# Performance work log

Measured on AMD Instinct MI355X. Metric: run time of the kernel, lower is better.

## Reference

```python
import jax, jax.numpy as jnp
import numpy as np

LN_EPS = 1e-5

def _layernorm(x, g, b):
    mu = jnp.mean(x, axis=-1, keepdims=True)
    var = jnp.mean(jnp.square(x - mu), axis=-1, keepdims=True)
    return (x - mu) * jax.lax.rsqrt(var + LN_EPS) * g + b

def setup_inputs() -> dict:
    key = jax.random.key(0)
    ks = jax.random.split(key, 8)
    B, T, C = 4, 2048, 1024
    s = 0.02
    return {
        "x": jax.random.normal(ks[0], (B, T, C), jnp.float32),
        "w_qkv": jax.random.normal(ks[1], (C, 3 * C), jnp.float32) * s,
        "b_qkv": jnp.zeros((3 * C,), jnp.float32),
        "w_out": jax.random.normal(ks[2], (C, C), jnp.float32) * s,
        "b_out": jnp.zeros((C,), jnp.float32),
        "w1": jax.random.normal(ks[3], (C, 4 * C), jnp.float32) * s,
        "b1": jnp.zeros((4 * C,), jnp.float32),
        "w2": jax.random.normal(ks[4], (4 * C, C), jnp.float32) * s,
        "b2": jnp.zeros((C,), jnp.float32),
        "g1": jnp.ones((C,), jnp.float32),
        "be1": jnp.zeros((C,), jnp.float32),
        "g2": jnp.ones((C,), jnp.float32),
        "be2": jnp.zeros((C,), jnp.float32),
        "n_head": 16,
    }

def reference(x, w_qkv, b_qkv, w_out, b_out, w1, b1, w2, b2, g1, be1, g2, be2, n_head):
    B, T, C = x.shape
    H = n_head
    D = C // H
    # --- causal self-attention ---
    qkv = x @ w_qkv + b_qkv                      # [B,T,3C]
    q, k, v = jnp.split(qkv, 3, axis=-1)
    q = q.reshape(B, T, H, D).transpose(0, 2, 1, 3)  # [B,H,T,D]
    k = k.reshape(B, T, H, D).transpose(0, 2, 1, 3)
    v = v.reshape(B, T, H, D).transpose(0, 2, 1, 3)
    attn = jnp.einsum("bhqd,bhkd->bhqk", q, k) * (1.0 / np.sqrt(D))
    causal = jnp.tril(jnp.ones((T, T), bool))
    attn = jnp.where(causal, attn, jnp.float32(-jnp.inf))
    attn = jax.nn.softmax(attn, axis=-1)
    y = jnp.einsum("bhqk,bhkd->bhqd", attn, v)
    y = y.transpose(0, 2, 1, 3).reshape(B, T, C)
    y = y @ w_out + b_out
    # post-norm residual (norm applied to sublayer output)
    x = x + _layernorm(y, g1, be1)
    # --- MLP ---
    h = jax.nn.gelu(x @ w1 + b1, approximate=False)
    h = h @ w2 + b2
    x = x + _layernorm(h, g2, be2)
    return x
```

## Files before the change

### kernel.cpp

```cpp
#include <hip/hip_runtime.h>
#include <hip/hip_bf16.h>

typedef unsigned short ushort_t;
using bf16x8 = __attribute__((ext_vector_type(8))) short;
using f32x4  = __attribute__((ext_vector_type(4))) float;

#define DEV __device__ __forceinline__

DEV unsigned short f2bf(float f) {
    unsigned int u = __builtin_bit_cast(unsigned int, f);
    u = (u + 0x7fffu + ((u >> 16) & 1u)) >> 16;
    return (unsigned short)u;
}

DEV int cvtpk_bf16(float lo, float hi) {
    int r;
    asm("v_cvt_pk_bf16_f32 %0, %1, %2" : "=v"(r) : "v"(lo), "v"(hi));
    return r;
}

DEV void gload16(const unsigned short* g, unsigned short* l) {
    __builtin_amdgcn_global_load_lds(
        (const __attribute__((address_space(1))) void*)g,
        (__attribute__((address_space(3))) void*)l, 16, 0, 0);
}

DEV float gelu_f(float v) {
    float u = v * (0.79788456f + 0.03567741f * v * v);
    float t = __builtin_amdgcn_exp2f(u * 2.88539008f);
    return v * t * __builtin_amdgcn_rcpf(t + 1.0f);
}

__global__ __launch_bounds__(256) void cvtbf_kernel(const float* __restrict__ in,
                                                    unsigned short* __restrict__ out) {
    int i = (blockIdx.x * 256 + threadIdx.x) * 4;
    float4 v = *(const float4*)&in[i];
    out[i + 0] = f2bf(v.x);
    out[i + 1] = f2bf(v.y);
    out[i + 2] = f2bf(v.z);
    out[i + 3] = f2bf(v.w);
}

__global__ __launch_bounds__(256) void transpose_cvt_kernel(const float* __restrict__ in,
                                                            unsigned short* __restrict__ out,
                                                            int R, int C) {
    __shared__ float t[32][33];
    int tx = threadIdx.x, ty = threadIdx.y;
    int c0 = blockIdx.x * 32, r0 = blockIdx.y * 32;
#pragma unroll
    for (int i = 0; i < 4; ++i)
        t[ty + i * 8][tx] = in[(size_t)(r0 + ty + i * 8) * C + c0 + tx];
    __syncthreads();
#pragma unroll
    for (int i = 0; i < 4; ++i)
        out[(size_t)(c0 + ty + i * 8) * R + r0 + tx] = f2bf(t[tx][ty + i * 8]);
}

__global__ __launch_bounds__(256) void vtrans_kernel(const unsigned short* __restrict__ qkvb,
                                                     unsigned short* __restrict__ vtg) {
    __shared__ unsigned short t[64 * 66];
    const int tid = threadIdx.x;
    const int t0 = blockIdx.x * 64;
    const int bh = blockIdx.y;
    const int b = bh >> 4, h = bh & 15;
    const unsigned short* src = qkvb + (size_t)(b * 2048 + t0) * 3072 + 2048 + h * 64;
#pragma unroll
    for (int c = 0; c < 2; ++c) {
        int cid = c * 256 + tid;
        int row = cid >> 3, cc = cid & 7;
        *(int4*)&t[row * 66 + cc * 8] = *(const int4*)&src[(size_t)row * 3072 + cc * 8];
    }
    __syncthreads();
    unsigned short* dst = vtg + (size_t)bh * 64 * 2048 + t0;
#pragma unroll
    for (int c = 0; c < 2; ++c) {
        int cid = c * 256 + tid;
        int d = cid >> 3, cc2 = cid & 7;
        bf16x8 v;
#pragma unroll
        for (int j = 0; j < 8; ++j) v[j] = (short)t[(cc2 * 8 + j) * 66 + d];
        *(bf16x8*)&dst[(size_t)d * 2048 + cc2 * 8] = v;
    }
}

template <int ACT, int OBF>
__global__ __launch_bounds__(512, 2) void gemm256_kernel(
    const unsigned short* __restrict__ A, const unsigned short* __restrict__ Bt,
    const float* __restrict__ bias, void* __restrict__ out,
    int N, int K, int gridNt) {
    __shared__ __align__(16) unsigned short lA[2][256 * 64];
    __shared__ __align__(16) unsigned short lB[2][256 * 64];
    const int tid = threadIdx.x;
    const int lane = tid & 63, wid = tid >> 6;
    const int g = lane >> 4, lr = lane & 15;
    const int wm = wid >> 2, wn = wid & 3;

    const int nwg = gridDim.x, cpx = nwg >> 3, bid = blockIdx.x;
    const int wkid = (bid & 7) * cpx + (bid >> 3);
    const int mt = wkid / gridNt, nt = wkid % gridNt;
    const int m0 = mt * 256, n0 = nt * 256;

    auto stageA = [&](int s, int kt, int bb) {
        int c = s * 512 + tid;
        int row = c & 255, kb = c >> 8;
        gload16(&A[(size_t)(m0 + row) * K + kt * 64 + kb * 8],
                &lA[bb][(size_t)(s * 512 + (tid & ~63)) * 8]);
    };
    auto stageB = [&](int s, int kt, int bb) {
        int c = s * 512 + tid;
        int row = c & 255, kb = c >> 8;
        gload16(&Bt[(size_t)(n0 + row) * K + kt * 64 + kb * 8],
                &lB[bb][(size_t)(s * 512 + (tid & ~63)) * 8]);
    };

    f32x4 acc[8][4] = {};
    bf16x8 bfr[4];
    const int nkt = K >> 6;

    stageA(0, 0, 0); stageA(1, 0, 0); stageB(0, 0, 0); stageB(1, 0, 0);
    stageA(2, 0, 0); stageA(3, 0, 0); stageB(2, 0, 0); stageB(3, 0, 0);
    asm volatile("s_waitcnt vmcnt(4)" ::: "memory");
    __builtin_amdgcn_s_barrier();
    asm volatile("" ::: "memory");

    for (int kt = 0; kt < nkt; ++kt) {
        const int buf = kt & 1;
        const bool more = (kt + 1 < nkt);
#pragma unroll
        for (int p = 0; p < 4; ++p) {
            const int ks = p >> 1, mh = p & 1;
            bf16x8 af[4];
#pragma unroll
            for (int mf2 = 0; mf2 < 4; ++mf2) {
                int c = (ks * 4 + g) * 256 + wm * 128 + (mh * 4 + mf2) * 16 + lr;
                af[mf2] = *(const bf16x8*)&lA[buf][(size_t)c * 8];
            }
            if (mh == 0) {
#pragma unroll
                for (int nf = 0; nf < 4; ++nf) {
                    int c = (ks * 4 + g) * 256 + wn * 64 + nf * 16 + lr;
                    bfr[nf] = *(const bf16x8*)&lB[buf][(size_t)c * 8];
                }
            }
            if (more) {
                if (p == 0)      { stageA(0, kt + 1, buf ^ 1); stageA(1, kt + 1, buf ^ 1); }
                else if (p == 1) { stageB(0, kt + 1, buf ^ 1); stageB(1, kt + 1, buf ^ 1); }
                else if (p == 2) { stageA(2, kt + 1, buf ^ 1); stageA(3, kt + 1, buf ^ 1); }
                else             { stageB(2, kt + 1, buf ^ 1); stageB(3, kt + 1, buf ^ 1); }
            }
            __builtin_amdgcn_s_barrier();
            asm volatile("s_waitcnt lgkmcnt(0)" ::: "memory");
            __builtin_amdgcn_sched_barrier(0);
            __builtin_amdgcn_s_setprio(1);
#pragma unroll
            for (int mf2 = 0; mf2 < 4; ++mf2)
#pragma unroll
                for (int nf = 0; nf < 4; ++nf)
                    acc[mh * 4 + mf2][nf] = __builtin_amdgcn_mfma_f32_16x16x32_bf16(
                        af[mf2], bfr[nf], acc[mh * 4 + mf2][nf], 0, 0, 0);
            __builtin_amdgcn_s_setprio(0);
            __builtin_amdgcn_sched_barrier(0);
            if (p == 1) {
                if (more) asm volatile("s_waitcnt vmcnt(4)" ::: "memory");
                else      asm volatile("s_waitcnt vmcnt(0)" ::: "memory");
            } else if (p == 3) {
                if (more) asm volatile("s_waitcnt vmcnt(4)" ::: "memory");
            }
            __builtin_amdgcn_s_barrier();
            asm volatile("" ::: "memory");
        }
    }

#pragma unroll
    for (int mf = 0; mf < 8; ++mf) {
#pragma unroll
        for (int nf = 0; nf < 4; ++nf) {
            int col = n0 + wn * 64 + nf * 16 + lr;
            float bv = bias[col];
#pragma unroll
            for (int r = 0; r < 4; ++r) {
                int row = m0 + wm * 128 + mf * 16 + g * 4 + r;
                float v = acc[mf][nf][r] + bv;
                if (ACT == 1) v = gelu_f(v);
                if (OBF)
                    ((unsigned short*)out)[(size_t)row * N + col] = f2bf(v);
                else
                    ((float*)out)[(size_t)row * N + col] = v;
            }
        }
    }
}

template <int ACT, int OBF>
__global__ __launch_bounds__(512, 2) void gemm128_kernel(
    const unsigned short* __restrict__ A, const unsigned short* __restrict__ Bt,
    const float* __restrict__ bias, void* __restrict__ out,
    int N, int K, int gridNt) {
    __shared__ __align__(16) unsigned short lA[2][128 * 64];
    __shared__ __align__(16) unsigned short lB[2][256 * 64];
    const int tid = threadIdx.x;
    const int lane = tid & 63, wid = tid >> 6;
    const int g = lane >> 4, lr = lane & 15;
    const int wm = wid >> 2, wn = wid & 3;

    const int nwg = gridDim.x, cpx = nwg >> 3, bid = blockIdx.x;
    const int wkid = (bid & 7) * cpx + (bid >> 3);
    const int mt = wkid / gridNt, nt = wkid % gridNt;
    const int m0 = mt * 128, n0 = nt * 256;

    auto stageA = [&](int s, int kt, int bb) {
        int c = s * 512 + tid;
        int row = c & 127, kb = c >> 7;
        gload16(&A[(size_t)(m0 + row) * K + kt * 64 + kb * 8],
                &lA[bb][(size_t)(s * 512 + (tid & ~63)) * 8]);
    };
    auto stageB = [&](int s, int kt, int bb) {
        int c = s * 512 + tid;
        int row = c & 255, kb = c >> 8;
        gload16(&Bt[(size_t)(n0 + row) * K + kt * 64 + kb * 8],
                &lB[bb][(size_t)(s * 512 + (tid & ~63)) * 8]);
    };

    f32x4 acc[4][4] = {};
    const int nkt = K >> 6;

    stageA(0, 0, 0); stageB(0, 0, 0); stageB(1, 0, 0);
    stageA(1, 0, 0); stageB(2, 0, 0); stageB(3, 0, 0);
    asm volatile("s_waitcnt vmcnt(3)" ::: "memory");
    __builtin_amdgcn_s_barrier();
    asm volatile("" ::: "memory");

    for (int kt = 0; kt < nkt; ++kt) {
        const int buf = kt & 1;
        const bool more = (kt + 1 < nkt);
#pragma unroll
        for (int ks = 0; ks < 2; ++ks) {
            bf16x8 af[4], bfr[4];
#pragma unroll
            for (int mf = 0; mf < 4; ++mf) {
                int c = (ks * 4 + g) * 128 + wm * 64 + mf * 16 + lr;
                af[mf] = *(const bf16x8*)&lA[buf][(size_t)c * 8];
            }
#pragma unroll
            for (int nf = 0; nf < 4; ++nf) {
                int c = (ks * 4 + g) * 256 + wn * 64 + nf * 16 + lr;
                bfr[nf] = *(const bf16x8*)&lB[buf][(size_t)c * 8];
            }
            if (more) {
                if (ks == 0) { stageA(0, kt + 1, buf ^ 1); stageB(0, kt + 1, buf ^ 1); stageB(1, kt + 1, buf ^ 1); }
                else         { stageA(1, kt + 1, buf ^ 1); stageB(2, kt + 1, buf ^ 1); stageB(3, kt + 1, buf ^ 1); }
            }
            __builtin_amdgcn_s_barrier();
            asm volatile("s_waitcnt lgkmcnt(0)" ::: "memory");
            __builtin_amdgcn_sched_barrier(0);
            __builtin_amdgcn_s_setprio(1);
#pragma unroll
            for (int mf = 0; mf < 4; ++mf)
#pragma unroll
                for (int nf = 0; nf < 4; ++nf)
                    acc[mf][nf] = __builtin_amdgcn_mfma_f32_16x16x32_bf16(
                        af[mf], bfr[nf], acc[mf][nf], 0, 0, 0);
            __builtin_amdgcn_s_setprio(0);
            __builtin_amdgcn_sched_barrier(0);
            if (ks == 0) {
                if (more) asm volatile("s_waitcnt vmcnt(3)" ::: "memory");
                else      asm volatile("s_waitcnt vmcnt(0)" ::: "memory");
            } else {
                if (more) asm volatile("s_waitcnt vmcnt(3)" ::: "memory");
            }
            __builtin_amdgcn_s_barrier();
            asm volatile("" ::: "memory");
        }
    }

#pragma unroll
    for (int mf = 0; mf < 4; ++mf) {
#pragma unroll
        for (int nf = 0; nf < 4; ++nf) {
            int col = n0 + wn * 64 + nf * 16 + lr;
            float bv = bias[col];
#pragma unroll
            for (int r = 0; r < 4; ++r) {
                int row = m0 + wm * 64 + mf * 16 + g * 4 + r;
                float v = acc[mf][nf][r] + bv;
                if (ACT == 1) v = gelu_f(v);
                if (OBF)
                    ((unsigned short*)out)[(size_t)row * N + col] = f2bf(v);
                else
                    ((float*)out)[(size_t)row * N + col] = v;
            }
        }
    }
}

__global__ __launch_bounds__(256) void attn_kernel(const unsigned short* __restrict__ qkv,
                                                   const unsigned short* __restrict__ vtg,
                                                   unsigned short* __restrict__ y) {
    __shared__ unsigned short Kl[2][4096];
    __shared__ unsigned short Vl[2][4096];
    const int tid = threadIdx.x, lane = tid & 63, w = tid >> 6;
    const int g = lane >> 4, lr = lane & 15;
    const int p = blockIdx.x, h = blockIdx.y, b = blockIdx.z;
    const int bh = b * 16 + h;
    const size_t rs3 = 3072;
    const unsigned short* qbase = qkv + (size_t)b * 2048 * rs3 + h * 64;
    const unsigned short* kbase = qbase + 1024;
    const unsigned short* vbase = vtg + (size_t)bh * 64 * 2048;

    int ksoff[2], vsoff[2], ldoff[2];
#pragma unroll
    for (int c = 0; c < 2; ++c) {
        int row = w * 16 + c * 8 + (lane >> 3);
        int ccs = (lane & 7) ^ (row & 7) ^ (row >> 3);
        ksoff[c] = row * 3072 + ccs * 8;
        vsoff[c] = row * 2048 + ccs * 8;
        ldoff[c] = (w * 16 + c * 8) * 64;
    }

    const int idxP0 = 4 * (32 * (g & 1) + lr);
    const int idxP1 = idxP0 + 64;
    int idxA[4];
#pragma unroll
    for (int r = 0; r < 4; ++r) idxA[r] = 4 * (g * 20 + r);
    const bool ghigh = (g >> 1) != 0;
    const float qscale = 0.125f * 1.44269504089f;

    auto process = [&](int J) {
        const int q0w = J * 128 + w * 32;
        const int ktend = 2 * J + 2;
#pragma unroll
        for (int c = 0; c < 2; ++c) {
            gload16(&kbase[ksoff[c]], &Kl[0][ldoff[c]]);
            gload16(&vbase[vsoff[c]], &Vl[0][ldoff[c]]);
        }
        int qf[2][2][4];
#pragma unroll
        for (int sub = 0; sub < 2; ++sub)
#pragma unroll
            for (int f = 0; f < 2; ++f) {
                int4 v = *(const int4*)&qbase[(size_t)(q0w + sub * 16 + lr) * rs3 + f * 32 + g * 8];
                int vv[4] = {v.x, v.y, v.z, v.w};
#pragma unroll
                for (int i = 0; i < 4; ++i) {
                    unsigned int u = (unsigned int)vv[i];
                    float lo = __builtin_bit_cast(float, u << 16) * qscale;
                    float hi = __builtin_bit_cast(float, u & 0xffff0000u) * qscale;
                    qf[sub][f][i] = cvtpk_bf16(lo, hi);
                }
            }

        f32x4 O[2][4] = {};
        float m_[2] = {-3.0e38f, -3.0e38f}, l_[2] = {0.f, 0.f};

        int buf = 0;
        for (int kt = 0; kt < ktend; ++kt) {
            asm volatile("s_waitcnt vmcnt(0)" ::: "memory");
            __builtin_amdgcn_s_barrier();
            asm volatile("" ::: "memory");
            if (kt + 1 < ktend) {
#pragma unroll
                for (int c = 0; c < 2; ++c) {
                    gload16(&kbase[(size_t)(kt + 1) * 64 * 3072 + ksoff[c]], &Kl[buf ^ 1][ldoff[c]]);
                    gload16(&vbase[vsoff[c] + (kt + 1) * 64], &Vl[buf ^ 1][ldoff[c]]);
                }
            }
            const unsigned short* Kc = Kl[buf];
            const unsigned short* Vc = Vl[buf];

            const bool act0 = (kt * 64) <= (q0w + 15);
            const bool act1 = (kt * 64) <= (q0w + 31);

            f32x4 s0[4], s1[4];
#pragma unroll
            for (int st = 0; st < 4; ++st) {
                int rbase = (st * 16 + lr) * 64;
                int sw = (lr & 7) ^ (st * 2 + (lr >> 3));
                bf16x8 kf0 = *(const bf16x8*)&Kc[rbase + ((g ^ sw) * 8)];
                bf16x8 kf1 = *(const bf16x8*)&Kc[rbase + (((4 + g) ^ sw) * 8)];
                if (act0) {
                    f32x4 a = {};
                    a = __builtin_amdgcn_mfma_f32_16x16x32_bf16(kf0, *(const bf16x8*)&qf[0][0], a, 0, 0, 0);
                    a = __builtin_amdgcn_mfma_f32_16x16x32_bf16(kf1, *(const bf16x8*)&qf[0][1], a, 0, 0, 0);
                    s0[st] = a;
                }
                if (act1) {
                    f32x4 a = {};
                    a = __builtin_amdgcn_mfma_f32_16x16x32_bf16(kf0, *(const bf16x8*)&qf[1][0], a, 0, 0, 0);
                    a = __builtin_amdgcn_mfma_f32_16x16x32_bf16(kf1, *(const bf16x8*)&qf[1][1], a, 0, 0, 0);
                    s1[st] = a;
                }
            }

            int wt0[2][4], wt1[2][4];
#pragma unroll
            for (int sub = 0; sub < 2; ++sub) {
                if (sub == 0 && !act0) continue;
                if (sub == 1 && !act1) continue;
                f32x4* s = (sub == 0) ? s0 : s1;
                const int qmin = q0w + sub * 16;
                if (kt * 64 + 63 > qmin) {
                    int qv = qmin + lr;
#pragma unroll
                    for (int st = 0; st < 4; ++st) {
                        int keyb = kt * 64 + st * 16 + g * 4;
#pragma unroll
                        for (int r = 0; r < 4; ++r)
                            if (keyb + r > qv) s[st][r] = -3.0e38f;
                    }
                }
                float mx = fmaxf(fmaxf(s[0][0], s[0][1]), fmaxf(s[0][2], s[0][3]));
#pragma unroll
                for (int st = 1; st < 4; ++st)
                    mx = fmaxf(mx, fmaxf(fmaxf(s[st][0], s[st][1]), fmaxf(s[st][2], s[st][3])));
                mx = fmaxf(mx, __shfl_xor(mx, 16));
                mx = fmaxf(mx, __shfl_xor(mx, 32));
                float mold = m_[sub];
                float mnew = fmaxf(mold, mx);
                float alpha = __builtin_amdgcn_exp2f(mold - mnew);
                m_[sub] = mnew;
                float rs = 0.f;
#pragma unroll
                for (int st = 0; st < 4; ++st)
#pragma unroll
                    for (int r = 0; r < 4; ++r) {
                        float pp = __builtin_amdgcn_exp2f(s[st][r] - mnew);
                        s[st][r] = pp;
                        rs += pp;
                    }
                rs += __shfl_xor(rs, 16);
                rs += __shfl_xor(rs, 32);
                l_[sub] = l_[sub] * alpha + rs;
                int av = __builtin_bit_cast(int, alpha);
                f32x4* Os = O[sub];
#pragma unroll
                for (int r = 0; r < 4; ++r) {
                    float ar = __builtin_bit_cast(float, __builtin_amdgcn_ds_bpermute(idxA[r], av));
#pragma unroll
                    for (int dt = 0; dt < 4; ++dt) Os[dt][r] *= ar;
                }
                int ws_[4][2];
#pragma unroll
                for (int st = 0; st < 4; ++st) {
                    ws_[st][0] = cvtpk_bf16(s[st][0], s[st][1]);
                    ws_[st][1] = cvtpk_bf16(s[st][2], s[st][3]);
                }
                int(*wt)[4] = (sub == 0) ? wt0 : wt1;
#pragma unroll
                for (int ks = 0; ks < 2; ++ks)
#pragma unroll
                    for (int hp = 0; hp < 4; ++hp) {
                        int idx = (hp < 2) ? idxP0 : idxP1;
                        int v0 = __builtin_amdgcn_ds_bpermute(idx, ws_[2 * ks][hp & 1]);
                        int v1 = __builtin_amdgcn_ds_bpermute(idx, ws_[2 * ks + 1][hp & 1]);
                        wt[ks][hp] = ghigh ? v1 : v0;
                    }
            }

#pragma unroll
            for (int ks = 0; ks < 2; ++ks) {
                bf16x8 pa0 = *(const bf16x8*)&wt0[ks][0];
                bf16x8 pa1 = *(const bf16x8*)&wt1[ks][0];
#pragma unroll
                for (int dt = 0; dt < 4; ++dt) {
                    int d = dt * 16 + lr;
                    int xv = (ks * 4 + g) ^ (lr & 7) ^ (dt * 2 + (lr >> 3));
                    bf16x8 vf = *(const bf16x8*)&Vc[d * 64 + xv * 8];
                    if (act0) O[0][dt] = __builtin_amdgcn_mfma_f32_16x16x32_bf16(pa0, vf, O[0][dt], 0, 0, 0);
                    if (act1) O[1][dt] = __builtin_amdgcn_mfma_f32_16x16x32_bf16(pa1, vf, O[1][dt], 0, 0, 0);
                }
            }
            buf ^= 1;
        }

#pragma unroll
        for (int sub = 0; sub < 2; ++sub) {
            int lv = __builtin_bit_cast(int, l_[sub]);
#pragma unroll
            for (int r = 0; r < 4; ++r) {
                float lval = __builtin_bit_cast(float, __builtin_amdgcn_ds_bpermute(idxA[r], lv));
                float inv = __builtin_amdgcn_rcpf(lval);
                int q = q0w + sub * 16 + g * 4 + r;
#pragma unroll
                for (int dt = 0; dt < 4; ++dt)
                    y[(size_t)(b * 2048 + q) * 1024 + h * 64 + dt * 16 + lr] =
                        f2bf(O[sub][dt][r] * inv);
            }
        }
    };

    process(15 - p);
    __syncthreads();
    process(p);
}

template <int WRITE_BF>
__global__ __launch_bounds__(256) void ln_kernel(const float* __restrict__ base,
                                                 const float* __restrict__ delta,
                                                 const float* __restrict__ gw,
                                                 const float* __restrict__ bw,
                                                 float* __restrict__ outf,
                                                 unsigned short* __restrict__ outb) {
    const int row = blockIdx.x;
    const int tid = threadIdx.x;
    const float* d = delta + (size_t)row * 1024;
    const float* bs = base + (size_t)row * 1024;
    float4 x = *(const float4*)&d[tid * 4];
    float s = x.x + x.y + x.z + x.w;
    float s2 = x.x * x.x + x.y * x.y + x.z * x.z + x.w * x.w;
#pragma unroll
    for (int off = 1; off < 64; off <<= 1) {
        s += __shfl_xor(s, off);
        s2 += __shfl_xor(s2, off);
    }
    __shared__ float red[8];
    if ((tid & 63) == 0) {
        red[tid >> 6] = s;
        red[4 + (tid >> 6)] = s2;
    }
    __syncthreads();
    s = red[0] + red[1] + red[2] + red[3];
    s2 = red[4] + red[5] + red[6] + red[7];
    float mu = s * (1.f / 1024.f);
    float var = s2 * (1.f / 1024.f) - mu * mu;
    float rsig = rsqrtf(var + 1e-5f);
    float4 bb = *(const float4*)&bs[tid * 4];
    float4 gv = *(const float4*)&gw[tid * 4];
    float4 bv = *(const float4*)&bw[tid * 4];
    float4 o;
    o.x = bb.x + (x.x - mu) * rsig * gv.x + bv.x;
    o.y = bb.y + (x.y - mu) * rsig * gv.y + bv.y;
    o.z = bb.z + (x.z - mu) * rsig * gv.z + bv.z;
    o.w = bb.w + (x.w - mu) * rsig * gv.w + bv.w;
    *(float4*)&outf[(size_t)row * 1024 + tid * 4] = o;
    if (WRITE_BF) {
        unsigned short* ob = outb + (size_t)row * 1024 + tid * 4;
        ob[0] = f2bf(o.x);
        ob[1] = f2bf(o.y);
        ob[2] = f2bf(o.z);
        ob[3] = f2bf(o.w);
    }
}

extern "C" void kernel_launch(void* const* d_in, const int* in_sizes, int n_in,
                              void* d_out, int out_size, void* d_ws, size_t ws_size,
                              hipStream_t stream) {
    const float* x = (const float*)d_in[0];
    const float* w_qkv = (const float*)d_in[1];
    const float* b_qkv = (const float*)d_in[2];
    const float* w_out = (const float*)d_in[3];
    const float* b_out = (const float*)d_in[4];
    const float* w1 = (const float*)d_in[5];
    const float* b1 = (const float*)d_in[6];
    const float* w2 = (const float*)d_in[7];
    const float* b2 = (const float*)d_in[8];
    const float* g1 = (const float*)d_in[9];
    const float* be1 = (const float*)d_in[10];
    const float* g2 = (const float*)d_in[11];
    const float* be2 = (const float*)d_in[12];

    const size_t MB = 1ull << 20;
    if (ws_size < 184 * MB) return;
    char* ws = (char*)d_ws;
    unsigned short* xb    = (unsigned short*)(ws + 0);
    unsigned short* vtg   = (unsigned short*)(ws + 0);
    unsigned short* wqkvt = (unsigned short*)(ws + 16 * MB);
    unsigned short* qkvb  = (unsigned short*)(ws + 22 * MB);
    unsigned short* hb    = (unsigned short*)(ws + 0);
    unsigned short* woutt = (unsigned short*)(ws + 70 * MB);
    unsigned short* yb    = (unsigned short*)(ws + 72 * MB);
    float*          attnp = (float*)(ws + 88 * MB);
    float*          ff    = (float*)(ws + 88 * MB);
    float*          x2f   = (float*)(ws + 120 * MB);
    unsigned short* x2b   = (unsigned short*)(ws + 152 * MB);
    unsigned short* w1t   = (unsigned short*)(ws + 168 * MB);
    unsigned short* w2t   = (unsigned short*)(ws + 176 * MB);

    cvtbf_kernel<<<8192, 256, 0, stream>>>(x, xb);
    transpose_cvt_kernel<<<dim3(96, 32), dim3(32, 8), 0, stream>>>(w_qkv, wqkvt, 1024, 3072);
    transpose_cvt_kernel<<<dim3(32, 32), dim3(32, 8), 0, stream>>>(w_out, woutt, 1024, 1024);
    transpose_cvt_kernel<<<dim3(128, 32), dim3(32, 8), 0, stream>>>(w1, w1t, 1024, 4096);
    transpose_cvt_kernel<<<dim3(32, 128), dim3(32, 8), 0, stream>>>(w2, w2t, 4096, 1024);
    gemm256_kernel<0, 1><<<384, 512, 0, stream>>>(xb, wqkvt, b_qkv, qkvb, 3072, 1024, 12);
    vtrans_kernel<<<dim3(32, 64), 256, 0, stream>>>(qkvb, vtg);
    attn_kernel<<<dim3(8, 16, 4), 256, 0, stream>>>(qkvb, vtg, yb);
    gemm128_kernel<0, 0><<<256, 512, 0, stream>>>(yb, woutt, b_out, attnp, 1024, 1024, 4);
    ln_kernel<1><<<8192, 256, 0, stream>>>(x, attnp, g1, be1, x2f, x2b);
    gemm256_kernel<1, 1><<<512, 512, 0, stream>>>(x2b, w1t, b1, hb, 4096, 1024, 16);
    gemm128_kernel<0, 0><<<256, 512, 0, stream>>>(hb, w2t, b2, ff, 1024, 4096, 4);
    ln_kernel<0><<<8192, 256, 0, stream>>>(x2f, ff, g2, be2, (float*)d_out, nullptr);
}
```

Measured before the change: 505.4 us.

## Enlarge attention KV tiles, add lazy softmax rescale, and group GEMM tile order

The attention kernel now works through 128-key K/V tiles instead of 64, with a new swizzled LDS layout. It drops the per-subtile activity checks and masks only on the diagonal tile. The online softmax rescales O and l only when the running max grows past a threshold, which saves the exp and bpermute work on most iterations. Blocks are remapped so each XCD handles contiguous batch-heads, and the GEMMs gain a grouped-M tile ordering for better L2 reuse. The costs are more LDS per block, some redundant MFMA work on fully masked subtiles, and numerics that depend on the rescale threshold being safe.

```diff
diff --git a/kernel.cpp b/kernel.cpp
--- a/kernel.cpp
+++ b/kernel.cpp
@@ -87,7 +87,7 @@
 __global__ __launch_bounds__(512, 2) void gemm256_kernel(
     const unsigned short* __restrict__ A, const unsigned short* __restrict__ Bt,
     const float* __restrict__ bias, void* __restrict__ out,
-    int N, int K, int gridNt) {
+    int N, int K, int gridNt, int GM) {
     __shared__ __align__(16) unsigned short lA[2][256 * 64];
     __shared__ __align__(16) unsigned short lB[2][256 * 64];
     const int tid = threadIdx.x;
@@ -97,7 +97,8 @@
 
     const int nwg = gridDim.x, cpx = nwg >> 3, bid = blockIdx.x;
     const int wkid = (bid & 7) * cpx + (bid >> 3);
-    const int mt = wkid / gridNt, nt = wkid % gridNt;
+    const int mt = (wkid / (GM * gridNt)) * GM + (wkid % GM);
+    const int nt = (wkid / GM) % gridNt;
     const int m0 = mt * 256, n0 = nt * 256;
 
     auto stageA = [&](int s, int kt, int bb) {
@@ -195,7 +196,7 @@
 __global__ __launch_bounds__(512, 2) void gemm128_kernel(
     const unsigned short* __restrict__ A, const unsigned short* __restrict__ Bt,
     const float* __restrict__ bias, void* __restrict__ out,
-    int N, int K, int gridNt) {
+    int N, int K, int gridNt, int GM) {
     __shared__ __align__(16) unsigned short lA[2][128 * 64];
     __shared__ __align__(16) unsigned short lB[2][256 * 64];
     const int tid = threadIdx.x;
@@ -205,7 +206,8 @@
 
     const int nwg = gridDim.x, cpx = nwg >> 3, bid = blockIdx.x;
     const int wkid = (bid & 7) * cpx + (bid >> 3);
-    const int mt = wkid / gridNt, nt = wkid % gridNt;
+    const int mt = (wkid / (GM * gridNt)) * GM + (wkid % GM);
+    const int nt = (wkid / GM) % gridNt;
     const int m0 = mt * 128, n0 = nt * 256;
 
     auto stageA = [&](int s, int kt, int bb) {
@@ -293,28 +295,32 @@
     }
 }
 
-__global__ __launch_bounds__(256) void attn_kernel(const unsigned short* __restrict__ qkv,
-                                                   const unsigned short* __restrict__ vtg,
-                                                   unsigned short* __restrict__ y) {
-    __shared__ unsigned short Kl[2][4096];
-    __shared__ unsigned short Vl[2][4096];
+__global__ __launch_bounds__(256, 2) void attn_kernel(const unsigned short* __restrict__ qkv,
+                                                      const unsigned short* __restrict__ vtg,
+                                                      unsigned short* __restrict__ y) {
+    __shared__ unsigned short Kl[2][128 * 64];
+    __shared__ unsigned short Vl[2][64 * 128];
     const int tid = threadIdx.x, lane = tid & 63, w = tid >> 6;
     const int g = lane >> 4, lr = lane & 15;
-    const int p = blockIdx.x, h = blockIdx.y, b = blockIdx.z;
-    const int bh = b * 16 + h;
+    const int id = blockIdx.x + 8 * (blockIdx.y + 16 * blockIdx.z);
+    const int xcd = id & 7, wrk = id >> 3;
+    const int bh = xcd * 8 + (wrk & 7);
+    const int p = wrk >> 3;
+    const int b = bh >> 4, h = bh & 15;
     const size_t rs3 = 3072;
     const unsigned short* qbase = qkv + (size_t)b * 2048 * rs3 + h * 64;
     const unsigned short* kbase = qbase + 1024;
     const unsigned short* vbase = vtg + (size_t)bh * 64 * 2048;
 
-    int ksoff[2], vsoff[2], ldoff[2];
-#pragma unroll
-    for (int c = 0; c < 2; ++c) {
-        int row = w * 16 + c * 8 + (lane >> 3);
-        int ccs = (lane & 7) ^ (row & 7) ^ (row >> 3);
-        ksoff[c] = row * 3072 + ccs * 8;
-        vsoff[c] = row * 2048 + ccs * 8;
-        ldoff[c] = (w * 16 + c * 8) * 64;
+    int ksoff[4], vsoff[4], ldoff[4];
+#pragma unroll
+    for (int c = 0; c < 4; ++c) {
+        int cid = c * 256 + tid;
+        int krow = cid >> 3, kcc = cid & 7;
+        ksoff[c] = krow * 3072 + (kcc ^ (krow & 7) ^ ((krow >> 3) & 7)) * 8;
+        int d = cid >> 4, tcs = cid & 15;
+        vsoff[c] = d * 2048 + (tcs ^ ((d & 7) ^ ((d >> 3) & 7))) * 8;
+        ldoff[c] = (c * 256 + (tid & ~63)) * 8;
     }
 
     const int idxP0 = 4 * (32 * (g & 1) + lr);
@@ -327,9 +333,9 @@
 
     auto process = [&](int J) {
         const int q0w = J * 128 + w * 32;
-        const int ktend = 2 * J + 2;
-#pragma unroll
-        for (int c = 0; c < 2; ++c) {
+        const int ktend = J + 1;
+#pragma unroll
+        for (int c = 0; c < 4; ++c) {
             gload16(&kbase[ksoff[c]], &Kl[0][ldoff[c]]);
             gload16(&vbase[vsoff[c]], &Vl[0][ldoff[c]]);
         }
@@ -359,50 +365,41 @@
             asm volatile("" ::: "memory");
             if (kt + 1 < ktend) {
 #pragma unroll
-                for (int c = 0; c < 2; ++c) {
-                    gload16(&kbase[(size_t)(kt + 1) * 64 * 3072 + ksoff[c]], &Kl[buf ^ 1][ldoff[c]]);
-                    gload16(&vbase[vsoff[c] + (kt + 1) * 64], &Vl[buf ^ 1][ldoff[c]]);
+                for (int c = 0; c < 4; ++c) {
+                    gload16(&kbase[(size_t)(kt + 1) * 128 * 3072 + ksoff[c]], &Kl[buf ^ 1][ldoff[c]]);
+                    gload16(&vbase[vsoff[c] + (kt + 1) * 128], &Vl[buf ^ 1][ldoff[c]]);
                 }
             }
             const unsigned short* Kc = Kl[buf];
             const unsigned short* Vc = Vl[buf];
 
-            const bool act0 = (kt * 64) <= (q0w + 15);
-            const bool act1 = (kt * 64) <= (q0w + 31);
-
-            f32x4 s0[4], s1[4];
-#pragma unroll
-            for (int st = 0; st < 4; ++st) {
+            f32x4 s0[8], s1[8];
+#pragma unroll
+            for (int st = 0; st < 8; ++st) {
                 int rbase = (st * 16 + lr) * 64;
-                int sw = (lr & 7) ^ (st * 2 + (lr >> 3));
+                int sw = (lr & 7) ^ ((st * 2 + (lr >> 3)) & 7);
                 bf16x8 kf0 = *(const bf16x8*)&Kc[rbase + ((g ^ sw) * 8)];
                 bf16x8 kf1 = *(const bf16x8*)&Kc[rbase + (((4 + g) ^ sw) * 8)];
-                if (act0) {
-                    f32x4 a = {};
-                    a = __builtin_amdgcn_mfma_f32_16x16x32_bf16(kf0, *(const bf16x8*)&qf[0][0], a, 0, 0, 0);
-                    a = __builtin_amdgcn_mfma_f32_16x16x32_bf16(kf1, *(const bf16x8*)&qf[0][1], a, 0, 0, 0);
-                    s0[st] = a;
-                }
-                if (act1) {
-                    f32x4 a = {};
-                    a = __builtin_amdgcn_mfma_f32_16x16x32_bf16(kf0, *(const bf16x8*)&qf[1][0], a, 0, 0, 0);
-                    a = __builtin_amdgcn_mfma_f32_16x16x32_bf16(kf1, *(const bf16x8*)&qf[1][1], a, 0, 0, 0);
-                    s1[st] = a;
-                }
-            }
-
-            int wt0[2][4], wt1[2][4];
+                f32x4 a = {};
+                a = __builtin_amdgcn_mfma_f32_16x16x32_bf16(kf0, *(const bf16x8*)&qf[0][0], a, 0, 0, 0);
+                a = __builtin_amdgcn_mfma_f32_16x16x32_bf16(kf1, *(const bf16x8*)&qf[0][1], a, 0, 0, 0);
+                s0[st] = a;
+                f32x4 c = {};
+                c = __builtin_amdgcn_mfma_f32_16x16x32_bf16(kf0, *(const bf16x8*)&qf[1][0], c, 0, 0, 0);
+                c = __builtin_amdgcn_mfma_f32_16x16x32_bf16(kf1, *(const bf16x8*)&qf[1][1], c, 0, 0, 0);
+                s1[st] = c;
+            }
+
+            int wt0[4][4], wt1[4][4];
 #pragma unroll
             for (int sub = 0; sub < 2; ++sub) {
-                if (sub == 0 && !act0) continue;
-                if (sub == 1 && !act1) continue;
                 f32x4* s = (sub == 0) ? s0 : s1;
                 const int qmin = q0w + sub * 16;
-                if (kt * 64 + 63 > qmin) {
+                if (kt == J) {
                     int qv = qmin + lr;
 #pragma unroll
-                    for (int st = 0; st < 4; ++st) {
-                        int keyb = kt * 64 + st * 16 + g * 4;
+                    for (int st = 0; st < 8; ++st) {
+                        int keyb = kt * 128 + st * 16 + g * 4;
 #pragma unroll
                         for (int r = 0; r < 4; ++r)
                             if (keyb + r > qv) s[st][r] = -3.0e38f;
@@ -410,43 +407,45 @@
                 }
                 float mx = fmaxf(fmaxf(s[0][0], s[0][1]), fmaxf(s[0][2], s[0][3]));
 #pragma unroll
-                for (int st = 1; st < 4; ++st)
+                for (int st = 1; st < 8; ++st)
                     mx = fmaxf(mx, fmaxf(fmaxf(s[st][0], s[st][1]), fmaxf(s[st][2], s[st][3])));
                 mx = fmaxf(mx, __shfl_xor(mx, 16));
                 mx = fmaxf(mx, __shfl_xor(mx, 32));
-                float mold = m_[sub];
-                float mnew = fmaxf(mold, mx);
-                float alpha = __builtin_amdgcn_exp2f(mold - mnew);
-                m_[sub] = mnew;
+                if (__any(mx - m_[sub] > 11.5f)) {
+                    float mnew = fmaxf(m_[sub], mx);
+                    float alpha = __builtin_amdgcn_exp2f(m_[sub] - mnew);
+                    m_[sub] = mnew;
+                    l_[sub] *= alpha;
+                    int av = __builtin_bit_cast(int, alpha);
+                    f32x4* Os = O[sub];
+#pragma unroll
+                    for (int r = 0; r < 4; ++r) {
+                        float ar = __builtin_bit_cast(float, __builtin_amdgcn_ds_bpermute(idxA[r], av));
+#pragma unroll
+                        for (int dt = 0; dt < 4; ++dt) Os[dt][r] *= ar;
+                    }
+                }
                 float rs = 0.f;
 #pragma unroll
-                for (int st = 0; st < 4; ++st)
+                for (int st = 0; st < 8; ++st)
 #pragma unroll
                     for (int r = 0; r < 4; ++r) {
-                        float pp = __builtin_amdgcn_exp2f(s[st][r] - mnew);
+                        float pp = __builtin_amdgcn_exp2f(s[st][r] - m_[sub]);
                         s[st][r] = pp;
                         rs += pp;
                     }
                 rs += __shfl_xor(rs, 16);
                 rs += __shfl_xor(rs, 32);
-                l_[sub] = l_[sub] * alpha + rs;
-                int av = __builtin_bit_cast(int, alpha);
-                f32x4* Os = O[sub];
-#pragma unroll
-                for (int r = 0; r < 4; ++r) {
-                    float ar = __builtin_bit_cast(float, __builtin_amdgcn_ds_bpermute(idxA[r], av));
-#pragma unroll
-                    for (int dt = 0; dt < 4; ++dt) Os[dt][r] *= ar;
-                }
-                int ws_[4][2];
-#pragma unroll
-                for (int st = 0; st < 4; ++st) {
+                l_[sub] += rs;
+                int ws_[8][2];
+#pragma unroll
+                for (int st = 0; st < 8; ++st) {
                     ws_[st][0] = cvtpk_bf16(s[st][0], s[st][1]);
                     ws_[st][1] = cvtpk_bf16(s[st][2], s[st][3]);
                 }
                 int(*wt)[4] = (sub == 0) ? wt0 : wt1;
 #pragma unroll
-                for (int ks = 0; ks < 2; ++ks)
+                for (int ks = 0; ks < 4; ++ks)
 #pragma unroll
                     for (int hp = 0; hp < 4; ++hp) {
                         int idx = (hp < 2) ? idxP0 : idxP1;
@@ -457,16 +456,16 @@
             }
 
 #pragma unroll
-            for (int ks = 0; ks < 2; ++ks) {
+            for (int ks = 0; ks < 4; ++ks) {
                 bf16x8 pa0 = *(const bf16x8*)&wt0[ks][0];
                 bf16x8 pa1 = *(const bf16x8*)&wt1[ks][0];
 #pragma unroll
                 for (int dt = 0; dt < 4; ++dt) {
                     int d = dt * 16 + lr;
-                    int xv = (ks * 4 + g) ^ (lr & 7) ^ (dt * 2 + (lr >> 3));
-                    bf16x8 vf = *(const bf16x8*)&Vc[d * 64 + xv * 8];
-                    if (act0) O[0][dt] = __builtin_amdgcn_mfma_f32_16x16x32_bf16(pa0, vf, O[0][dt], 0, 0, 0);
-                    if (act1) O[1][dt] = __builtin_amdgcn_mfma_f32_16x16x32_bf16(pa1, vf, O[1][dt], 0, 0, 0);
+                    int tc = (ks * 4 + g) ^ ((lr & 7) ^ ((dt * 2 + (lr >> 3)) & 7));
+                    bf16x8 vf = *(const bf16x8*)&Vc[d * 128 + tc * 8];
+                    O[0][dt] = __builtin_amdgcn_mfma_f32_16x16x32_bf16(pa0, vf, O[0][dt], 0, 0, 0);
+                    O[1][dt] = __builtin_amdgcn_mfma_f32_16x16x32_bf16(pa1, vf, O[1][dt], 0, 0, 0);
                 }
             }
             buf ^= 1;
@@ -580,12 +579,12 @@
     transpose_cvt_kernel<<<dim3(32, 32), dim3(32, 8), 0, stream>>>(w_out, woutt, 1024, 1024);
     transpose_cvt_kernel<<<dim3(128, 32), dim3(32, 8), 0, stream>>>(w1, w1t, 1024, 4096);
     transpose_cvt_kernel<<<dim3(32, 128), dim3(32, 8), 0, stream>>>(w2, w2t, 4096, 1024);
-    gemm256_kernel<0, 1><<<384, 512, 0, stream>>>(xb, wqkvt, b_qkv, qkvb, 3072, 1024, 12);
+    gemm256_kernel<0, 1><<<384, 512, 0, stream>>>(xb, wqkvt, b_qkv, qkvb, 3072, 1024, 12, 4);
     vtrans_kernel<<<dim3(32, 64), 256, 0, stream>>>(qkvb, vtg);
     attn_kernel<<<dim3(8, 16, 4), 256, 0, stream>>>(qkvb, vtg, yb);
-    gemm128_kernel<0, 0><<<256, 512, 0, stream>>>(yb, woutt, b_out, attnp, 1024, 1024, 4);
+    gemm128_kernel<0, 0><<<256, 512, 0, stream>>>(yb, woutt, b_out, attnp, 1024, 1024, 4, 8);
     ln_kernel<1><<<8192, 256, 0, stream>>>(x, attnp, g1, be1, x2f, x2b);
-    gemm256_kernel<1, 1><<<512, 512, 0, stream>>>(x2b, w1t, b1, hb, 4096, 1024, 16);
-    gemm128_kernel<0, 0><<<256, 512, 0, stream>>>(hb, w2t, b2, ff, 1024, 4096, 4);
+    gemm256_kernel<1, 1><<<512, 512, 0, stream>>>(x2b, w1t, b1, hb, 4096, 1024, 16, 4);
+    gemm128_kernel<0, 0><<<256, 512, 0, stream>>>(hb, w2t, b2, ff, 1024, 4096, 4, 8);
     ln_kernel<0><<<8192, 256, 0, stream>>>(x2f, ff, g2, be2, (float*)d_out, nullptr);
 }
```

After: 471.0 us. 1.07x faster.
